# Optimization experiments

Measured on AMD Instinct MI355X. Metric: run time of the kernel, lower is better.

Reference implementation:

```python
import jax, jax.numpy as jnp
import numpy as np

B, NPG = 128, 512            # graphs, nodes per graph (batch is contiguous & uniform)
N = B * NPG                  # 65536 nodes
DEG = 8
E = N * DEG                  # 524288 edges
F_IN, NHID = 128, 64
H, C = 3, NHID               # GAT heads, out channels per head
HC = H * C                   # 192
NCLS = 10
RATIO = 0.5
NEG_SLOPE = 0.2


def setup_inputs() -> dict:
    key = jax.random.key(0)
    ks = jax.random.split(key, 24)
    x = jax.random.normal(ks[0], (N, F_IN), jnp.float32)
    # edges constrained within each graph (graphs are contiguous blocks of NPG nodes)
    offs = jnp.repeat(jnp.arange(B, dtype=jnp.int32) * NPG, NPG * DEG)
    src = jax.random.randint(ks[1], (E,), 0, NPG, dtype=jnp.int32) + offs
    dst = jax.random.randint(ks[2], (E,), 0, NPG, dtype=jnp.int32) + offs
    edge_index = jnp.stack([src, dst], axis=0)
    edge_attr = jax.random.normal(ks[3], (E, 2), jnp.float32)
    batch = jnp.repeat(jnp.arange(B, dtype=jnp.int32), NPG)

    def lin(k, o, i):
        return jax.random.normal(k, (o, i), jnp.float32) / np.float32(np.sqrt(i))

    return {
        "x": x, "edge_index": edge_index, "edge_attr": edge_attr, "batch": batch,
        # lin: num_features -> nhid//2
        "W_lin": lin(ks[4], NHID // 2, F_IN), "b_lin": jnp.zeros((NHID // 2,), jnp.float32),
        # GATConv(nhid//2 -> nhid, heads=3, edge_dim=2)
        "W_src": lin(ks[5], HC, NHID // 2),
        "att_src": jax.random.normal(ks[6], (H, C), jnp.float32) / np.float32(np.sqrt(C)),
        "att_dst": jax.random.normal(ks[7], (H, C), jnp.float32) / np.float32(np.sqrt(C)),
        "W_edge": lin(ks[8], HC, 2),
        "att_edge": jax.random.normal(ks[9], (H, C), jnp.float32) / np.float32(np.sqrt(C)),
        "b_gat": jnp.zeros((HC,), jnp.float32),
        # SAGPool score layer: GCNConv(nhid*3 -> 1)
        "W_gcn": lin(ks[10], 1, HC), "b_gcn": jnp.zeros((1,), jnp.float32),
        # classifier MLP
        "W1": lin(ks[11], NHID, 2 * HC), "b1": jnp.zeros((NHID,), jnp.float32),
        "W2": lin(ks[12], NHID // 2, NHID), "b2": jnp.zeros((NHID // 2,), jnp.float32),
        "W3": lin(ks[13], NCLS, NHID // 2), "b3": jnp.zeros((NCLS,), jnp.float32),
    }


def reference(x, edge_index, edge_attr, batch,
              W_lin, b_lin, W_src, att_src, att_dst, W_edge, att_edge, b_gat,
              W_gcn, b_gcn, W1, b1, W2, b2, W3, b3):
    src, dst = edge_index[0], edge_index[1]

    # ---- lin + ELU -------------------------------------------------------
    h = jax.nn.elu(x @ W_lin.T + b_lin)                       # [N, nhid//2]

    # ---- GATConv(heads=3, edge_dim=2), add_self_loops fill_value='mean' --
    loop = jnp.arange(N, dtype=src.dtype)
    cnt = jax.ops.segment_sum(jnp.ones((E,), h.dtype), dst, num_segments=N)
    loop_attr = jax.ops.segment_sum(edge_attr, dst, num_segments=N) / jnp.maximum(cnt, 1.0)[:, None]
    s_full = jnp.concatenate([src, loop])
    d_full = jnp.concatenate([dst, loop])
    ea_full = jnp.concatenate([edge_attr, loop_attr], axis=0)  # [E+N, 2]

    xp = (h @ W_src.T).reshape(N, H, C)                        # projected per-head feats
    a_src = (xp * att_src).sum(-1)                             # [N, H]
    a_dst = (xp * att_dst).sum(-1)                             # [N, H]
    ef = (ea_full @ W_edge.T).reshape(-1, H, C)
    a_edge = (ef * att_edge).sum(-1)                           # [E+N, H]

    alpha = jax.nn.leaky_relu(a_src[s_full] + a_dst[d_full] + a_edge, NEG_SLOPE)
    m = jax.ops.segment_max(alpha, d_full, num_segments=N)     # scatter-softmax over dst
    ealpha = jnp.exp(alpha - m[d_full])
    denom = jax.ops.segment_sum(ealpha, d_full, num_segments=N)
    alpha = ealpha / (denom[d_full] + 1e-16)                   # [E+N, H]

    out = jax.ops.segment_sum(alpha[:, :, None] * xp[s_full], d_full, num_segments=N)
    x1 = jax.nn.relu(out.reshape(N, HC) + b_gat)               # [N, 192]

    # ---- SAGPool: GCNConv score + per-graph top-k (mask form) ------------
    xw = x1 @ W_gcn.T                                          # [N, 1]
    deg = jax.ops.segment_sum(jnp.ones((E,), x1.dtype), dst, num_segments=N) + 1.0
    dinv = jax.lax.rsqrt(deg)
    agg = jax.ops.segment_sum((dinv[src] * dinv[dst])[:, None] * xw[src], dst, num_segments=N)
    score = (agg + (dinv ** 2)[:, None] * xw + b_gcn)[:, 0]    # [N]

    k = int(np.ceil(RATIO * NPG))                              # nodes kept per graph
    s2 = score.reshape(B, NPG)
    rank = jnp.argsort(jnp.argsort(-s2, axis=1), axis=1)
    mask = rank < k                                            # [B, NPG] top-k selection

    xs = (x1 * jnp.tanh(score)[:, None]).reshape(B, NPG, HC)
    gmp = jnp.max(jnp.where(mask[:, :, None], xs, -jnp.inf), axis=1)   # [B, 192]
    gap = jnp.sum(jnp.where(mask[:, :, None], xs, 0.0), axis=1) / k    # [B, 192]
    r = jnp.concatenate([gmp, gap], axis=1)                    # [B, 384]

    # ---- classifier MLP (dropout is identity in eval) ---------------------
    r = jax.nn.relu(r @ W1.T + b1)
    r = jax.nn.relu(r @ W2.T + b2)
    return jax.nn.log_softmax(r @ W3.T + b3, axis=-1)          # [B, num_classes]
```

## Files before the change

### kernel.cpp

```cpp
#include <hip/hip_runtime.h>
#include <hip/hip_bf16.h>
#include <math.h>

#define NN   65536
#define EE   524288
#define BB   128
#define NPGC 512
#define HCC  192
#define KSEL 256
#define NEG  0.2f
#define PSEG 8
#define SEGN (NPGC / PSEG)
#define MAXD 40
#define SLOTS ((size_t)NN * MAXD)
#define EPG   4096

__device__ __forceinline__ int nodeblock_base(int bx) {
    int xcd = bx & 7, j = bx >> 3;
    int g = xcd + 8 * (j >> 1);
    return g * NPGC + (j & 1) * 256;
}

__global__ __launch_bounds__(256) void k_h(
    const float* __restrict__ x, const float* __restrict__ W_lin,
    const float* __restrict__ b_lin, float* __restrict__ hbuf) {
    __shared__ float Wl[128 * 16];
    int t = threadIdx.x;
    int half = blockIdx.y;
#pragma unroll
    for (int i = 0; i < 8; ++i) {
        int idx = t + i * 256;
        int k = idx >> 4, jj = idx & 15;
        Wl[idx] = W_lin[(half * 16 + jj) * 128 + k];
    }
    __syncthreads();
    int n = nodeblock_base(blockIdx.x) + t;
    const float4* xr = (const float4*)(x + (size_t)n * 128);
    float acc[16];
#pragma unroll
    for (int j = 0; j < 16; ++j) acc[j] = b_lin[half * 16 + j];
#pragma unroll 4
    for (int q = 0; q < 32; ++q) {
        float4 a = xr[q];
        const float* w = &Wl[(q * 4) * 16];
#pragma unroll
        for (int j = 0; j < 16; ++j) {
            acc[j] += a.x * w[j] + a.y * w[16 + j] +
                      a.z * w[32 + j] + a.w * w[48 + j];
        }
    }
#pragma unroll
    for (int j = 0; j < 16; ++j)
        acc[j] = acc[j] > 0.f ? acc[j] : expm1f(acc[j]);
    float4* dst = (float4*)(hbuf + (size_t)n * 32 + half * 16);
#pragma unroll
    for (int q = 0; q < 4; ++q)
        dst[q] = make_float4(acc[4 * q], acc[4 * q + 1],
                             acc[4 * q + 2], acc[4 * q + 3]);
}

__global__ __launch_bounds__(256) void k_xp(
    const float* __restrict__ hbuf, const float* __restrict__ W_src,
    const float* __restrict__ att_src, const float* __restrict__ att_dst,
    float* __restrict__ xp, float* __restrict__ ap_s, float* __restrict__ ap_d) {
    __shared__ float Ws[32 * 33];
    int t = threadIdx.x;
    int h = blockIdx.y;
    int ch = blockIdx.z;
    {
        int rowbase = (h * 64 + ch * 32) * 32;
#pragma unroll
        for (int i = 0; i < 4; ++i) {
            int idx = t + i * 256;
            int r = idx >> 5, k = idx & 31;
            Ws[k * 33 + r] = W_src[rowbase + idx];
        }
    }
    __syncthreads();
    int n = nodeblock_base(blockIdx.x) + t;
    const float4* hr = (const float4*)(hbuf + (size_t)n * 32);
    float acc[32];
#pragma unroll
    for (int c = 0; c < 32; ++c) acc[c] = 0.f;
#pragma unroll
    for (int q = 0; q < 8; ++q) {
        float4 hv = hr[q];
        const float* w = &Ws[(q * 4) * 33];
#pragma unroll
        for (int c = 0; c < 32; ++c) {
            acc[c] += hv.x * w[c] + hv.y * w[33 + c] +
                      hv.z * w[66 + c] + hv.w * w[99 + c];
        }
    }
    float as = 0.f, ad = 0.f;
    const float* ats = att_src + h * 64 + ch * 32;
    const float* atd = att_dst + h * 64 + ch * 32;
#pragma unroll
    for (int c = 0; c < 32; ++c) {
        as += acc[c] * ats[c];
        ad += acc[c] * atd[c];
    }
    ap_s[(size_t)(ch * 3 + h) * NN + n] = as;
    ap_d[(size_t)(ch * 3 + h) * NN + n] = ad;
    float4* dst = (float4*)(xp + (size_t)n * HCC + h * 64 + ch * 32);
#pragma unroll
    for (int q = 0; q < 8; ++q)
        dst[q] = make_float4(acc[4 * q], acc[4 * q + 1],
                             acc[4 * q + 2], acc[4 * q + 3]);
}

__global__ __launch_bounds__(1024) void k_edges(
    const int* __restrict__ ei, const float* __restrict__ ea,
    const float* __restrict__ ap_s, const float* __restrict__ ap_d,
    const float* __restrict__ W_edge, const float* __restrict__ att_edge,
    int* __restrict__ fill, float4* __restrict__ slotA) {
    __shared__ int   s_cnt[NPGC], s_pos[NPGC];
    __shared__ float s_la[NPGC * 2];
    __shared__ float s_as[NPGC * 3], s_ad[NPGC * 3];
    __shared__ float s_ac[6];
    int b = blockIdx.x, t = threadIdx.x;
    int g = (b & 7) + 8 * (b >> 3);
    int nbase = g * NPGC;
    int ebase = g * EPG;
    if (t < NPGC) { s_cnt[t] = 0; s_pos[t] = 0; }
    s_la[t] = 0.f;
    if (t < 6) s_ac[t] = 0.f;
    for (int i = t; i < NPGC * 3; i += 1024) {
        int h = i >> 9, nl = i & (NPGC - 1);
        s_as[nl * 3 + h] = ap_s[(size_t)h * NN + nbase + nl] +
                           ap_s[(size_t)(3 + h) * NN + nbase + nl];
        s_ad[nl * 3 + h] = ap_d[(size_t)h * NN + nbase + nl] +
                           ap_d[(size_t)(3 + h) * NN + nbase + nl];
    }
    __syncthreads();
    if (t < 192) {
        float ae = att_edge[t];
        int h = t >> 6;
        atomicAdd(&s_ac[h],     W_edge[2 * t]     * ae);
        atomicAdd(&s_ac[3 + h], W_edge[2 * t + 1] * ae);
    }
#pragma unroll
    for (int k = 0; k < 4; ++k) {
        int e = ebase + t + k * 1024;
        int dl = ei[EE + e] & (NPGC - 1);
        atomicAdd(&s_cnt[dl], 1);
        atomicAdd(&s_la[2 * dl],     ea[2 * e]);
        atomicAdd(&s_la[2 * dl + 1], ea[2 * e + 1]);
    }
    __syncthreads();
    float ac[6];
#pragma unroll
    for (int h = 0; h < 6; ++h) ac[h] = s_ac[h];
    if (t < NPGC) {
        int cnt = s_cnt[t];
        int n = nbase + t;
        fill[n] = cnt;
        float inv = 1.f / fmaxf((float)cnt, 1.f);
        float l0 = s_la[2 * t] * inv, l1 = s_la[2 * t + 1] * inv;
        float v[3];
#pragma unroll
        for (int h = 0; h < 3; ++h) {
            float a = s_as[t * 3 + h] + s_ad[t * 3 + h] +
                      l0 * ac[h] + l1 * ac[3 + h];
            v[h] = a >= 0.f ? a : NEG * a;
        }
        slotA[(size_t)n * MAXD] = make_float4(v[0], v[1], v[2],
                                              __int_as_float(n));
    }
#pragma unroll
    for (int k = 0; k < 4; ++k) {
        int e = ebase + t + k * 1024;
        int s = ei[e], d = ei[EE + e];
        int sl = s & (NPGC - 1), dl = d & (NPGC - 1);
        float e0 = ea[2 * e], e1 = ea[2 * e + 1];
        float v[3];
#pragma unroll
        for (int h = 0; h < 3; ++h) {
            float a = s_as[sl * 3 + h] + s_ad[dl * 3 + h] +
                      e0 * ac[h] + e1 * ac[3 + h];
            v[h] = a >= 0.f ? a : NEG * a;
        }
        int pos = atomicAdd(&s_pos[dl], 1);
        if (pos < MAXD - 1)
            slotA[(size_t)d * MAXD + 1 + pos] =
                make_float4(v[0], v[1], v[2], __int_as_float(s));
    }
}

__global__ __launch_bounds__(256) void k_agg(
    const int* __restrict__ fill, const float4* __restrict__ slotA,
    const float* __restrict__ xp,
    const float* __restrict__ b_gat, const float* __restrict__ W_gcn,
    float* __restrict__ x1, float* __restrict__ xwd, float* __restrict__ dinv) {
    __shared__ float4 wsl[4][64];
    int wave = threadIdx.x >> 6, lane = threadIdx.x & 63;
    int b = blockIdx.x;
    int xcd = b & 7, j = b >> 3;
    int g = (j >> 7) * 8 + xcd;
    int n = g * NPGC + (j & 127) * 4 + wave;

    int ctrue = fill[n];
    int cnt = ctrue < (MAXD - 1) ? ctrue : (MAXD - 1);
    int tot = cnt + 1;

    float4 ent = make_float4(0.f, 0.f, 0.f, 0.f);
    if (lane < tot) {
        float4 pk = slotA[(size_t)n * MAXD + lane];
        ent = make_float4(__expf(pk.x), __expf(pk.y), __expf(pk.z), pk.w);
    }
    wsl[wave][lane] = ent;

    int head = lane >> 4;
    bool act = lane < 48;
    const float4* xp4 = (const float4*)xp;
    float ax = 0.f, ay = 0.f, az = 0.f, aw = 0.f, den = 0.f;
    int s = 0;
    for (; s + 3 < tot; s += 4) {
        float4 eA = wsl[wave][s],     eB = wsl[wave][s + 1];
        float4 eC = wsl[wave][s + 2], eD = wsl[wave][s + 3];
        float wA = head == 0 ? eA.x : (head == 1 ? eA.y : eA.z);
        float wB = head == 0 ? eB.x : (head == 1 ? eB.y : eB.z);
        float wC = head == 0 ? eC.x : (head == 1 ? eC.y : eC.z);
        float wD = head == 0 ? eD.x : (head == 1 ? eD.y : eD.z);
        den += (wA + wB) + (wC + wD);
        if (act) {
            float4 vA = xp4[(size_t)__float_as_int(eA.w) * 48 + lane];
            float4 vB = xp4[(size_t)__float_as_int(eB.w) * 48 + lane];
            float4 vC = xp4[(size_t)__float_as_int(eC.w) * 48 + lane];
            float4 vD = xp4[(size_t)__float_as_int(eD.w) * 48 + lane];
            ax += wA * vA.x + wB * vB.x + wC * vC.x + wD * vD.x;
            ay += wA * vA.y + wB * vB.y + wC * vC.y + wD * vD.y;
            az += wA * vA.z + wB * vB.z + wC * vC.z + wD * vD.z;
            aw += wA * vA.w + wB * vB.w + wC * vC.w + wD * vD.w;
        }
    }
    for (; s < tot; ++s) {
        float4 eA = wsl[wave][s];
        float wA = head == 0 ? eA.x : (head == 1 ? eA.y : eA.z);
        den += wA;
        if (act) {
            float4 vA = xp4[(size_t)__float_as_int(eA.w) * 48 + lane];
            ax += wA * vA.x; ay += wA * vA.y; az += wA * vA.z; aw += wA * vA.w;
        }
    }
    float p = 0.f;
    if (act) {
        float id = 1.f / (den + 1e-16f);
        float4 bg = ((const float4*)b_gat)[lane];
        float4 v;
        v.x = fmaxf(ax * id + bg.x, 0.f);
        v.y = fmaxf(ay * id + bg.y, 0.f);
        v.z = fmaxf(az * id + bg.z, 0.f);
        v.w = fmaxf(aw * id + bg.w, 0.f);
        ((float4*)x1)[(size_t)n * 48 + lane] = v;
        float4 wg = ((const float4*)W_gcn)[lane];
        p = v.x * wg.x + v.y * wg.y + v.z * wg.z + v.w * wg.w;
    }
#pragma unroll
    for (int msk = 32; msk > 0; msk >>= 1) p += __shfl_xor(p, msk, 64);
    if (lane == 0) {
        float dv = rsqrtf((float)ctrue + 1.f);
        xwd[n] = p * dv;
        dinv[n] = dv;
    }
}

__global__ __launch_bounds__(256) void k_score(
    const int* __restrict__ fill, const float4* __restrict__ slotA,
    const float* __restrict__ xwd, const float* __restrict__ dinv,
    const float* __restrict__ b_gcn, float* __restrict__ score) {
    int wave = threadIdx.x >> 6, lane = threadIdx.x & 63;
    int b = blockIdx.x;
    int xcd = b & 7, j = b >> 3;
    int g = (j >> 7) * 8 + xcd;
    int n = g * NPGC + (j & 127) * 4 + wave;

    int ctrue = fill[n];
    int cnt = ctrue < (MAXD - 1) ? ctrue : (MAXD - 1);
    float acc = 0.f;
    if (lane <= cnt) {
        int src = __float_as_int(
            ((const float*)slotA)[((size_t)n * MAXD + lane) * 4 + 3]);
        acc = xwd[src];
    }
#pragma unroll
    for (int msk = 32; msk > 0; msk >>= 1) acc += __shfl_xor(acc, msk, 64);
    if (lane == 0) score[n] = b_gcn[0] + dinv[n] * acc;
}

__global__ __launch_bounds__(192) void k_poolrank(
    const float* __restrict__ score, const float* __restrict__ x1,
    float* __restrict__ pmax, float* __restrict__ psum) {
    __shared__ float sc[NPGC];
    __shared__ float ts_s[SEGN];
    __shared__ int sel_s[SEGN];
    int b = blockIdx.x;
    int xcd = b & 7, gslot = (b >> 3) & 15, seg = b >> 7;
    int g = gslot * 8 + xcd;
    int t = threadIdx.x;
    int gbase = g * NPGC;
    for (int i = t; i < NPGC; i += 192) sc[i] = score[gbase + i];
    __syncthreads();
    if (t < SEGN) {
        int iloc = seg * SEGN + t;
        float si = sc[iloc];
        int rank = 0;
        for (int j = 0; j < NPGC; ++j) {
            float sj = sc[j];
            rank += (sj > si) || (sj == si && j < iloc);
        }
        sel_s[t] = (rank < KSEL) ? 1 : 0;
        ts_s[t] = tanhf(si);
    }
    __syncthreads();
    int nb = gbase + seg * SEGN;
    float mx = -1e30f, sm = 0.f;
    for (int i = 0; i < SEGN; ++i) {
        if (sel_s[i]) {
            float v = x1[(size_t)(nb + i) * HCC + t] * ts_s[i];
            mx = fmaxf(mx, v);
            sm += v;
        }
    }
    size_t pb = (size_t)(g * PSEG + seg) * HCC + t;
    pmax[pb] = mx;
    psum[pb] = sm;
}

__global__ __launch_bounds__(384) void k_mlp(
    const float* __restrict__ pmax, const float* __restrict__ psum,
    const float* __restrict__ W1, const float* __restrict__ b1,
    const float* __restrict__ W2, const float* __restrict__ b2,
    const float* __restrict__ W3, const float* __restrict__ b3,
    float* __restrict__ out) {
    __shared__ float rs[384], part[384], h1[64], h2[32], lg[10], mls;
    int g = blockIdx.x, t = threadIdx.x;
    if (t < HCC) {
        float mx = -1e30f, sm = 0.f;
#pragma unroll
        for (int s = 0; s < PSEG; ++s) {
            mx = fmaxf(mx, pmax[(size_t)(g * PSEG + s) * HCC + t]);
            sm += psum[(size_t)(g * PSEG + s) * HCC + t];
        }
        rs[t] = mx;
        rs[HCC + t] = sm * (1.f / (float)KSEL);
    }
    __syncthreads();
    {
        int o = t / 6, sl = t - o * 6;
        const float* wr = W1 + o * 384 + sl * 64;
        const float* rr = rs + sl * 64;
        float s = 0.f;
#pragma unroll 8
        for (int k = 0; k < 64; ++k) s += rr[k] * wr[k];
        part[t] = s;
    }
    __syncthreads();
    if (t < 64) {
        float s = b1[t];
#pragma unroll
        for (int j = 0; j < 6; ++j) s += part[t * 6 + j];
        h1[t] = fmaxf(s, 0.f);
    }
    __syncthreads();
    if (t < 256) {
        int o = t >> 3, sl = t & 7;
        const float* wr = W2 + o * 64 + sl * 8;
        const float* hr = h1 + sl * 8;
        float s = 0.f;
#pragma unroll
        for (int k = 0; k < 8; ++k) s += hr[k] * wr[k];
        part[t] = s;
    }
    __syncthreads();
    if (t < 32) {
        float s = b2[t];
#pragma unroll
        for (int j = 0; j < 8; ++j) s += part[t * 8 + j];
        h2[t] = fmaxf(s, 0.f);
    }
    __syncthreads();
    if (t < 10) {
        float s = b3[t];
        for (int k = 0; k < 32; ++k) s += h2[k] * W3[t * 32 + k];
        lg[t] = s;
    }
    __syncthreads();
    if (t == 0) {
        float mx = lg[0];
        for (int j = 1; j < 10; ++j) mx = fmaxf(mx, lg[j]);
        float se = 0.f;
        for (int j = 0; j < 10; ++j) se += expf(lg[j] - mx);
        mls = mx + logf(se);
    }
    __syncthreads();
    if (t < 10) out[g * 10 + t] = lg[t] - mls;
}

extern "C" void kernel_launch(void* const* d_in, const int* in_sizes, int n_in,
                              void* d_out, int out_size, void* d_ws, size_t ws_size,
                              hipStream_t stream) {
    const float* x        = (const float*)d_in[0];
    const int*   ei       = (const int*)d_in[1];
    const float* ea       = (const float*)d_in[2];
    const float* W_lin    = (const float*)d_in[4];
    const float* b_lin    = (const float*)d_in[5];
    const float* W_src    = (const float*)d_in[6];
    const float* att_src  = (const float*)d_in[7];
    const float* att_dst  = (const float*)d_in[8];
    const float* W_edge   = (const float*)d_in[9];
    const float* att_edge = (const float*)d_in[10];
    const float* b_gat    = (const float*)d_in[11];
    const float* W_gcn    = (const float*)d_in[12];
    const float* b_gcn    = (const float*)d_in[13];
    const float* W1 = (const float*)d_in[14]; const float* b1 = (const float*)d_in[15];
    const float* W2 = (const float*)d_in[16]; const float* b2 = (const float*)d_in[17];
    const float* W3 = (const float*)d_in[18]; const float* b3 = (const float*)d_in[19];
    float* out = (float*)d_out;

    char* ws = (char*)d_ws;
    size_t off = 0;
    auto alloc = [&](size_t bytes) {
        size_t r = off;
        off += (bytes + 255) & ~(size_t)255;
        return r;
    };
    float* xp      = (float*)(ws + alloc((size_t)NN * HCC * 4));
    float* x1      = (float*)(ws + alloc((size_t)NN * HCC * 4));
    float* hbuf    = (float*)(ws + alloc((size_t)NN * 32 * 4));
    int*   fill    = (int*)(ws + alloc((size_t)NN * 4));
    float* ap_s    = (float*)(ws + alloc((size_t)NN * 6 * 4));
    float* ap_d    = (float*)(ws + alloc((size_t)NN * 6 * 4));
    float4* slotA  = (float4*)(ws + alloc(SLOTS * 16));
    float* xwd     = (float*)(ws + alloc((size_t)NN * 4));
    float* dinv    = (float*)(ws + alloc((size_t)NN * 4));
    float* score   = (float*)(ws + alloc((size_t)NN * 4));
    float* pmax    = (float*)(ws + alloc((size_t)BB * PSEG * HCC * 4));
    float* psum    = (float*)(ws + alloc((size_t)BB * PSEG * HCC * 4));

    k_h<<<dim3(256, 2), 256, 0, stream>>>(x, W_lin, b_lin, hbuf);
    k_xp<<<dim3(256, 3, 2), 256, 0, stream>>>(hbuf, W_src, att_src, att_dst,
                                              xp, ap_s, ap_d);
    k_edges<<<BB, 1024, 0, stream>>>(ei, ea, ap_s, ap_d, W_edge, att_edge,
                                     fill, slotA);
    k_agg<<<NN / 4, 256, 0, stream>>>(fill, slotA, xp, b_gat, W_gcn,
                                      x1, xwd, dinv);
    k_score<<<NN / 4, 256, 0, stream>>>(fill, slotA, xwd, dinv, b_gcn, score);
    k_poolrank<<<BB * PSEG, 192, 0, stream>>>(score, x1, pmax, psum);
    k_mlp<<<BB, 384, 0, stream>>>(pmax, psum, W1, b1, W2, b2, W3, b3, out);
}
```

Measured before the change: 264.4 us.

## Fuse edge count and slot-fill passes; per-head LDS weight layout in aggregation

Merges the two passes over each graph's edges in k_edges into one. The slot-position atomic counter now doubles as the in-degree count, removing the separate s_cnt array and its atomics. Edge indices and attributes are loaded once with vector int4/float4 loads instead of scalar re-reads. In k_agg, the exp-weights are stored per head as float2 (weight, src) in shared memory so each lane reads its own head's weight directly, replacing the per-edge select chain and narrowing the LDS reads. A wave's inactive lanes (lane >= 48) still read head 0's entries, and the self-loop slot write now happens after the edge slots.

```diff
diff --git a/kernel.cpp b/kernel.cpp
--- a/kernel.cpp
+++ b/kernel.cpp
@@ -114,7 +114,7 @@
     const float* __restrict__ ap_s, const float* __restrict__ ap_d,
     const float* __restrict__ W_edge, const float* __restrict__ att_edge,
     int* __restrict__ fill, float4* __restrict__ slotA) {
-    __shared__ int   s_cnt[NPGC], s_pos[NPGC];
+    __shared__ int   s_pos[NPGC];
     __shared__ float s_la[NPGC * 2];
     __shared__ float s_as[NPGC * 3], s_ad[NPGC * 3];
     __shared__ float s_ac[6];
@@ -122,7 +122,7 @@
     int g = (b & 7) + 8 * (b >> 3);
     int nbase = g * NPGC;
     int ebase = g * EPG;
-    if (t < NPGC) { s_cnt[t] = 0; s_pos[t] = 0; }
+    if (t < NPGC) s_pos[t] = 0;
     s_la[t] = 0.f;
     if (t < 6) s_ac[t] = 0.f;
     for (int i = t; i < NPGC * 3; i += 1024) {
@@ -139,20 +139,41 @@
         atomicAdd(&s_ac[h],     W_edge[2 * t]     * ae);
         atomicAdd(&s_ac[3 + h], W_edge[2 * t + 1] * ae);
     }
+    int4  se  = ((const int4*)(ei + ebase))[t];
+    int4  de  = ((const int4*)(ei + EE + ebase))[t];
+    float4 a0 = ((const float4*)(ea + 2 * ebase))[2 * t];
+    float4 a1 = ((const float4*)(ea + 2 * ebase))[2 * t + 1];
+    __syncthreads();
+    float ac[6];
+#pragma unroll
+    for (int h = 0; h < 6; ++h) ac[h] = s_ac[h];
+
+    int   ss[4] = {se.x, se.y, se.z, se.w};
+    int   dd[4] = {de.x, de.y, de.z, de.w};
+    float e0v[4] = {a0.x, a0.z, a1.x, a1.z};
+    float e1v[4] = {a0.y, a0.w, a1.y, a1.w};
 #pragma unroll
     for (int k = 0; k < 4; ++k) {
-        int e = ebase + t + k * 1024;
-        int dl = ei[EE + e] & (NPGC - 1);
-        atomicAdd(&s_cnt[dl], 1);
-        atomicAdd(&s_la[2 * dl],     ea[2 * e]);
-        atomicAdd(&s_la[2 * dl + 1], ea[2 * e + 1]);
-    }
-    __syncthreads();
-    float ac[6];
-#pragma unroll
-    for (int h = 0; h < 6; ++h) ac[h] = s_ac[h];
+        int s = ss[k], d = dd[k];
+        int sl = s & (NPGC - 1), dl = d & (NPGC - 1);
+        float e0 = e0v[k], e1 = e1v[k];
+        atomicAdd(&s_la[2 * dl],     e0);
+        atomicAdd(&s_la[2 * dl + 1], e1);
+        float v[3];
+#pragma unroll
+        for (int h = 0; h < 3; ++h) {
+            float a = s_as[sl * 3 + h] + s_ad[dl * 3 + h] +
+                      e0 * ac[h] + e1 * ac[3 + h];
+            v[h] = a >= 0.f ? a : NEG * a;
+        }
+        int pos = atomicAdd(&s_pos[dl], 1);
+        if (pos < MAXD - 1)
+            slotA[(size_t)(nbase + dl) * MAXD + 1 + pos] =
+                make_float4(v[0], v[1], v[2], __int_as_float(s));
+    }
+    __syncthreads();
     if (t < NPGC) {
-        int cnt = s_cnt[t];
+        int cnt = s_pos[t];
         int n = nbase + t;
         fill[n] = cnt;
         float inv = 1.f / fmaxf((float)cnt, 1.f);
@@ -167,24 +188,6 @@
         slotA[(size_t)n * MAXD] = make_float4(v[0], v[1], v[2],
                                               __int_as_float(n));
     }
-#pragma unroll
-    for (int k = 0; k < 4; ++k) {
-        int e = ebase + t + k * 1024;
-        int s = ei[e], d = ei[EE + e];
-        int sl = s & (NPGC - 1), dl = d & (NPGC - 1);
-        float e0 = ea[2 * e], e1 = ea[2 * e + 1];
-        float v[3];
-#pragma unroll
-        for (int h = 0; h < 3; ++h) {
-            float a = s_as[sl * 3 + h] + s_ad[dl * 3 + h] +
-                      e0 * ac[h] + e1 * ac[3 + h];
-            v[h] = a >= 0.f ? a : NEG * a;
-        }
-        int pos = atomicAdd(&s_pos[dl], 1);
-        if (pos < MAXD - 1)
-            slotA[(size_t)d * MAXD + 1 + pos] =
-                make_float4(v[0], v[1], v[2], __int_as_float(s));
-    }
 }
 
 __global__ __launch_bounds__(256) void k_agg(
@@ -192,7 +195,7 @@
     const float* __restrict__ xp,
     const float* __restrict__ b_gat, const float* __restrict__ W_gcn,
     float* __restrict__ x1, float* __restrict__ xwd, float* __restrict__ dinv) {
-    __shared__ float4 wsl[4][64];
+    __shared__ float2 wsl[4][3][64];
     int wave = threadIdx.x >> 6, lane = threadIdx.x & 63;
     int b = blockIdx.x;
     int xcd = b & 7, j = b >> 3;
@@ -203,44 +206,40 @@
     int cnt = ctrue < (MAXD - 1) ? ctrue : (MAXD - 1);
     int tot = cnt + 1;
 
-    float4 ent = make_float4(0.f, 0.f, 0.f, 0.f);
     if (lane < tot) {
         float4 pk = slotA[(size_t)n * MAXD + lane];
-        ent = make_float4(__expf(pk.x), __expf(pk.y), __expf(pk.z), pk.w);
-    }
-    wsl[wave][lane] = ent;
-
-    int head = lane >> 4;
+        wsl[wave][0][lane] = make_float2(__expf(pk.x), pk.w);
+        wsl[wave][1][lane] = make_float2(__expf(pk.y), pk.w);
+        wsl[wave][2][lane] = make_float2(__expf(pk.z), pk.w);
+    }
     bool act = lane < 48;
+    int head = act ? (lane >> 4) : 0;
+    const float2* wp = wsl[wave][head];
     const float4* xp4 = (const float4*)xp;
     float ax = 0.f, ay = 0.f, az = 0.f, aw = 0.f, den = 0.f;
     int s = 0;
     for (; s + 3 < tot; s += 4) {
-        float4 eA = wsl[wave][s],     eB = wsl[wave][s + 1];
-        float4 eC = wsl[wave][s + 2], eD = wsl[wave][s + 3];
-        float wA = head == 0 ? eA.x : (head == 1 ? eA.y : eA.z);
-        float wB = head == 0 ? eB.x : (head == 1 ? eB.y : eB.z);
-        float wC = head == 0 ? eC.x : (head == 1 ? eC.y : eC.z);
-        float wD = head == 0 ? eD.x : (head == 1 ? eD.y : eD.z);
-        den += (wA + wB) + (wC + wD);
+        float2 wsA = wp[s],     wsB = wp[s + 1];
+        float2 wsC = wp[s + 2], wsD = wp[s + 3];
+        den += (wsA.x + wsB.x) + (wsC.x + wsD.x);
         if (act) {
-            float4 vA = xp4[(size_t)__float_as_int(eA.w) * 48 + lane];
-            float4 vB = xp4[(size_t)__float_as_int(eB.w) * 48 + lane];
-            float4 vC = xp4[(size_t)__float_as_int(eC.w) * 48 + lane];
-            float4 vD = xp4[(size_t)__float_as_int(eD.w) * 48 + lane];
-            ax += wA * vA.x + wB * vB.x + wC * vC.x + wD * vD.x;
-            ay += wA * vA.y + wB * vB.y + wC * vC.y + wD * vD.y;
-            az += wA * vA.z + wB * vB.z + wC * vC.z + wD * vD.z;
-            aw += wA * vA.w + wB * vB.w + wC * vC.w + wD * vD.w;
+            float4 vA = xp4[(size_t)__float_as_int(wsA.y) * 48 + lane];
+            float4 vB = xp4[(size_t)__float_as_int(wsB.y) * 48 + lane];
+            float4 vC = xp4[(size_t)__float_as_int(wsC.y) * 48 + lane];
+            float4 vD = xp4[(size_t)__float_as_int(wsD.y) * 48 + lane];
+            ax += wsA.x * vA.x + wsB.x * vB.x + wsC.x * vC.x + wsD.x * vD.x;
+            ay += wsA.x * vA.y + wsB.x * vB.y + wsC.x * vC.y + wsD.x * vD.y;
+            az += wsA.x * vA.z + wsB.x * vB.z + wsC.x * vC.z + wsD.x * vD.z;
+            aw += wsA.x * vA.w + wsB.x * vB.w + wsC.x * vC.w + wsD.x * vD.w;
         }
     }
     for (; s < tot; ++s) {
-        float4 eA = wsl[wave][s];
-        float wA = head == 0 ? eA.x : (head == 1 ? eA.y : eA.z);
-        den += wA;
+        float2 wsA = wp[s];
+        den += wsA.x;
         if (act) {
-            float4 vA = xp4[(size_t)__float_as_int(eA.w) * 48 + lane];
-            ax += wA * vA.x; ay += wA * vA.y; az += wA * vA.z; aw += wA * vA.w;
+            float4 vA = xp4[(size_t)__float_as_int(wsA.y) * 48 + lane];
+            ax += wsA.x * vA.x; ay += wsA.x * vA.y;
+            az += wsA.x * vA.z; aw += wsA.x * vA.w;
         }
     }
     float p = 0.f;
```

Result: no change. 262.1 us (-0.9%).
